# Performance work log

Hardware: AMD Instinct MI355X
Metric: run time of the kernel (lower is better)

## Reference

```python
import jax, jax.numpy as jnp
import numpy as np

NKV = 8      # n_head_kv
G = 8        # n_head // n_head_kv
D = 64       # head_dim (hardcoded in source views)
NH = NKV * G # n_head = 64


def rotate_half(x):
    x1, x2 = x[..., : D // 2], x[..., D // 2:]
    return jnp.concatenate((-x2, x1), axis=-1)


def setup_inputs() -> dict:
    key = jax.random.key(0)
    ks = jax.random.split(key, 9)
    B, S, H = 2, 1024, 4096
    hidden_states = jax.random.normal(ks[0], (B, S, H), dtype=jnp.float32)
    alibi = jnp.zeros((B * NH, 1, S), dtype=jnp.float32)            # unused in this forward path
    attention_mask = jnp.zeros((B, 1, S, S), dtype=jnp.float32)      # unused (is_causal=True)
    cos = jax.random.uniform(ks[1], (S, D), dtype=jnp.float32, minval=-1.0, maxval=1.0)
    sin = jax.random.uniform(ks[2], (S, D), dtype=jnp.float32, minval=-1.0, maxval=1.0)
    wq = jax.random.normal(ks[3], (H, H), dtype=jnp.float32) * 0.02          # Linear weight (out, in)
    wk = jax.random.normal(ks[4], (NKV * D, H), dtype=jnp.float32) * 0.02
    wv = jax.random.normal(ks[5], (NKV * D, H), dtype=jnp.float32) * 0.02
    wd = jax.random.normal(ks[6], (H, H), dtype=jnp.float32) * 0.02          # dense weight
    return {"hidden_states": hidden_states, "alibi": alibi, "attention_mask": attention_mask,
            "cos": cos, "sin": sin, "wq": wq, "wk": wk, "wv": wv, "wd": wd}


def reference(hidden_states, alibi, attention_mask, cos, sin, wq, wk, wv, wd):
    B, S, H = hidden_states.shape
    # fused-style projections (Linear: x @ W.T, no bias)
    # q: [B, S, NKV, G, D] -> [B, NKV, G, S, D]; head h = kv_group*G + j (group-major, matches source rearrange)
    q = (hidden_states @ wq.T).reshape(B, S, NKV, G, D).transpose(0, 2, 3, 1, 4)
    k = (hidden_states @ wk.T).reshape(B, S, NKV, D).transpose(0, 2, 1, 3)   # [B, NKV, S, D]
    v = (hidden_states @ wv.T).reshape(B, S, NKV, D).transpose(0, 2, 1, 3)
    # RoPE (cos/sin broadcast over batch/head dims)
    q = q * cos + rotate_half(q) * sin
    k = k * cos + rotate_half(k) * sin
    # grouped-query attention without materializing broadcast K/V
    inv_norm = jnp.asarray(1.0 / np.sqrt(D), dtype=hidden_states.dtype)
    scores = jnp.einsum('bkgsd,bktd->bkgst', q, k) * inv_norm        # [B, NKV, G, S, S]
    causal = jnp.tril(jnp.ones((S, S), dtype=bool))
    neg = jnp.finfo(scores.dtype).min
    scores = jnp.where(causal, scores, scores + neg)
    probs = jax.nn.softmax(scores, axis=-1)
    out = jnp.einsum('bkgst,bktd->bkgsd', probs, v)                  # [B, NKV, G, S, D]
    out = out.reshape(B, NH, S, D).transpose(0, 2, 1, 3).reshape(B, S, NH * D)
    return out @ wd.T
```

## Files before the change

### kernel.cpp

```cpp
#include <hip/hip_runtime.h>
#include <hip/hip_bf16.h>
#include <cstdint>

typedef short short8 __attribute__((ext_vector_type(8)));
typedef __bf16 bf16x8 __attribute__((ext_vector_type(8)));
typedef float float4v __attribute__((ext_vector_type(4)));
typedef float float16v __attribute__((ext_vector_type(16)));

#define NKV 8
#define G 8
#define D 64
#define NH 64
#define BB 2
#define S 1024
#define H 4096
#define MROWS (BB*S)
#define NQKV (H + 2*NKV*D)

__device__ __forceinline__ unsigned short f2b(float f) {
    union { float f; uint32_t u; } v; v.f = f;
    uint32_t u = v.u;
    uint32_t r = (u + 0x7FFFu + ((u >> 16) & 1u)) >> 16;
    return (unsigned short)r;
}
__device__ __forceinline__ float b2f(unsigned short b) {
    union { float f; uint32_t u; } v; v.u = ((uint32_t)b) << 16;
    return v.f;
}
__device__ __forceinline__ unsigned short f2b_n(float f) {
    union { __bf16 h; unsigned short u; } v; v.h = (__bf16)f;
    return v.u;
}

__device__ __forceinline__ void gload_lds16(const unsigned short* g, unsigned short* l) {
    __builtin_amdgcn_global_load_lds(
        (const __attribute__((address_space(1))) uint32_t*)g,
        (__attribute__((address_space(3))) uint32_t*)l, 16, 0, 0);
}

__global__ void cvt_all(const float* __restrict__ hs, const float* __restrict__ wq,
                        const float* __restrict__ wk, const float* __restrict__ wv,
                        const float* __restrict__ wd,
                        unsigned short* __restrict__ hs_b, unsigned short* __restrict__ wqkv_b,
                        unsigned short* __restrict__ wd_b) {
    const size_t N0 = (size_t)MROWS * H;
    const size_t N1 = (size_t)H * H;
    const size_t N2 = (size_t)512 * H;
    const size_t N3 = (size_t)512 * H;
    const size_t N4 = (size_t)H * H;
    const size_t total4 = (N0 + N1 + N2 + N3 + N4) / 4;
    size_t i = (size_t)blockIdx.x * blockDim.x + threadIdx.x;
    const size_t stride = (size_t)gridDim.x * blockDim.x;
    for (; i < total4; i += stride) {
        size_t e = i * 4;
        const float* s; unsigned short* d;
        if (e < N0)                { s = hs + e;                  d = hs_b + e; }
        else if (e < N0+N1)        { s = wq + (e-N0);             d = wqkv_b + (e-N0); }
        else if (e < N0+N1+N2)     { s = wk + (e-N0-N1);          d = wqkv_b + N1 + (e-N0-N1); }
        else if (e < N0+N1+N2+N3)  { s = wv + (e-N0-N1-N2);       d = wqkv_b + N1+N2 + (e-N0-N1-N2); }
        else                       { s = wd + (e-N0-N1-N2-N3);    d = wd_b + (e-N0-N1-N2-N3); }
        float4 f = *(const float4*)s;
        ushort4 o;
        o.x = f2b(f.x); o.y = f2b(f.y); o.z = f2b(f.z); o.w = f2b(f.w);
        *(ushort4*)d = o;
    }
}

template <int MODE>
__global__ __launch_bounds__(256) void gemm_nt(
    const unsigned short* __restrict__ A, const unsigned short* __restrict__ W,
    void* __restrict__ Cv, int M, int N, int K,
    const float* __restrict__ cosb, const float* __restrict__ sinb,
    unsigned short* __restrict__ qa, unsigned short* __restrict__ ka,
    unsigned short* __restrict__ vt) {
    __shared__ unsigned short sh[17408];
    unsigned short* As = sh;
    unsigned short* Bs = sh + 4096;
    const int bm = blockIdx.y * 128, bn = blockIdx.x * 128;
    const int tid = threadIdx.x;
    const int w = tid >> 6, lane = tid & 63;
    const int n32 = lane & 31, khalf = lane >> 5;
    const int wm = (w & 1) * 64, wn = (w >> 1) * 64;

    const int r0 = tid >> 2;
    const int c0 = (tid & 3) ^ ((r0 >> 2) & 3);
    const unsigned short* pA0 = A + (size_t)(bm + r0) * K + c0 * 8;
    const unsigned short* pA1 = A + (size_t)(bm + r0 + 64) * K + c0 * 8;
    const unsigned short* pW0 = W + (size_t)(bn + r0) * K + c0 * 8;
    const unsigned short* pW1 = W + (size_t)(bn + r0 + 64) * K + c0 * 8;
    unsigned short* Asl0 = As + tid * 8;
    unsigned short* Asl1 = As + 2048 + tid * 8;
    unsigned short* Bsl0 = Bs + tid * 8;
    unsigned short* Bsl1 = Bs + 2048 + tid * 8;

    const unsigned short* aP[2][2];
    const unsigned short* bP[2][2];
#pragma unroll
    for (int g = 0; g < 2; g++)
#pragma unroll
        for (int s = 0; s < 2; s++) {
            int cp = ((s << 1) | khalf) ^ ((n32 >> 2) & 3);
            aP[g][s] = &As[(wm + g * 32 + n32) * 32 + cp * 8];
            bP[g][s] = &Bs[(wn + g * 32 + n32) * 32 + cp * 8];
        }

    float16v acc[2][2] = {};

    const int iters = K >> 5;
    for (int it = 0; it < iters; ++it) {
        __syncthreads();
        gload_lds16(pA0, Asl0);
        gload_lds16(pA1, Asl1);
        gload_lds16(pW0, Bsl0);
        gload_lds16(pW1, Bsl1);
        pA0 += 32; pA1 += 32; pW0 += 32; pW1 += 32;
        __syncthreads();
        bf16x8 af[2][2], bf[2][2];
#pragma unroll
        for (int g = 0; g < 2; g++)
#pragma unroll
            for (int s = 0; s < 2; s++) {
                af[g][s] = *(const bf16x8*)aP[g][s];
                bf[g][s] = *(const bf16x8*)bP[g][s];
            }
#pragma unroll
        for (int s = 0; s < 2; s++)
#pragma unroll
            for (int mg = 0; mg < 2; mg++)
#pragma unroll
                for (int ng = 0; ng < 2; ng++)
                    acc[mg][ng] = __builtin_amdgcn_mfma_f32_32x32x16_bf16(
                        af[mg][s], bf[ng][s], acc[mg][ng], 0, 0, 0);
    }

    if (MODE == 0) {
#pragma unroll
        for (int mg = 0; mg < 2; mg++) {
#pragma unroll
            for (int ng = 0; ng < 2; ng++) {
                int gcol = bn + wn + ng * 32 + n32;
#pragma unroll
                for (int reg = 0; reg < 16; reg++) {
                    int grow = bm + wm + mg * 32 + (reg & 3) + 8 * (reg >> 2) + 4 * khalf;
                    ((float*)Cv)[(size_t)grow * N + gcol] = acc[mg][ng][reg];
                }
            }
        }
    } else {
        const int colbase = bn + wn;
        const float SCQ = 0.125f * 1.44269504089f;
        if (bn < H + 512) {
#pragma unroll
            for (int mg = 0; mg < 2; mg++) {
#pragma unroll
                for (int reg = 0; reg < 16; reg++) {
                    int grow = bm + wm + mg * 32 + (reg & 3) + 8 * (reg >> 2) + 4 * khalf;
                    int s = grow & 1023, b = grow >> 10;
                    float x0 = acc[mg][0][reg], x1 = acc[mg][1][reg];
                    float c0  = cosb[s * 64 + n32],      sn0 = sinb[s * 64 + n32];
                    float c1  = cosb[s * 64 + 32 + n32], sn1 = sinb[s * 64 + 32 + n32];
                    float y0 = x0 * c0 - x1 * sn0;
                    float y1 = x1 * c1 + x0 * sn1;
                    unsigned short* dp;
                    if (bn < H) {
                        y0 *= SCQ; y1 *= SCQ;
                        dp = qa + (size_t)(b * 64 + (colbase >> 6)) * (S * D) + s * 64 + n32;
                    } else {
                        dp = ka + (size_t)(b * 8 + ((colbase - H) >> 6)) * (S * D) + s * 64 + n32;
                    }
                    dp[0] = f2b(y0); dp[32] = f2b(y1);
                }
            }
        } else {
            __syncthreads();
#pragma unroll
            for (int mg = 0; mg < 2; mg++)
#pragma unroll
                for (int ng = 0; ng < 2; ng++)
#pragma unroll
                    for (int reg = 0; reg < 16; reg++) {
                        int cl = wn + ng * 32 + n32;
                        int rl = wm + mg * 32 + (reg & 3) + 8 * (reg >> 2) + 4 * khalf;
                        sh[cl * 136 + rl] = f2b(acc[mg][ng][reg]);
                    }
            __syncthreads();
            {
                const int bb = bm >> 10, s0 = bm & 1023;
                const int kv0 = (bn - (H + 512)) >> 6;
                const int cl = tid >> 1, shalf = (tid & 1) * 64;
                const int kv = kv0 + (cl >> 6), dd = cl & 63;
                unsigned short* dstp = vt + (size_t)(bb * 8 + kv) * (D * S)
                                          + (size_t)dd * S + s0 + shalf;
                const unsigned short* srcp = sh + cl * 136 + shalf;
#pragma unroll
                for (int j = 0; j < 8; j++)
                    *(short8*)(dstp + j * 8) = *(const short8*)(srcp + j * 8);
            }
        }
    }
}

__global__ __launch_bounds__(256, 2) void attn_kernel(
    const unsigned short* __restrict__ qa, const unsigned short* __restrict__ ka,
    const unsigned short* __restrict__ vt, unsigned short* __restrict__ out) {
    __shared__ unsigned short Ps[4 * 16 * 72];
    const int p = blockIdx.x;
    const int yy = blockIdx.y;
    const int b = yy >> 5, kvh = (yy >> 2) & 7, gp = yy & 3;
    const int h0 = b * 64 + kvh * 8 + gp * 2;
    const int tid = threadIdx.x, w = tid >> 6, lane = tid & 63;
    const int col = lane & 15, quad = lane >> 4;
    const unsigned short* Kg = ka + (size_t)(b * NKV + kvh) * (S * D);
    const unsigned short* Vg = vt + (size_t)(b * NKV + kvh) * (D * S);
    float4v zero4 = {0.f, 0.f, 0.f, 0.f};

    const int qt0 = p, qt1 = 15 - p;
    const int qb[2] = {qt0 * 64, qt1 * 64};

    bf16x8 aq[2][2][2];
#pragma unroll
    for (int part = 0; part < 2; part++)
#pragma unroll
        for (int hd = 0; hd < 2; hd++)
#pragma unroll
            for (int c = 0; c < 2; c++)
                aq[part][hd][c] = *(const bf16x8*)&qa[(size_t)(h0 + hd) * (S * D)
                                    + (size_t)qb[part] * D + (w * 16 + col) * 64 + c * 32 + quad * 8];

    float l_run[2][2][4] = {};
    float4v o_acc[2][2][4];
#pragma unroll
    for (int part = 0; part < 2; part++)
#pragma unroll
        for (int hd = 0; hd < 2; hd++)
#pragma unroll
            for (int dg = 0; dg < 4; dg++) o_acc[part][hd][dg] = zero4;

    for (int kt = 0; kt <= qt1; kt++) {
        const int kb = kt * 64;
        bf16x8 bk[4][2], bv[4][2];
#pragma unroll
        for (int n16 = 0; n16 < 4; n16++) {
            const unsigned short* kr = &Kg[(size_t)(kb + n16 * 16 + col) * 64 + quad * 8];
            bk[n16][0] = *(const bf16x8*)kr;
            bk[n16][1] = *(const bf16x8*)(kr + 32);
        }
#pragma unroll
        for (int dg = 0; dg < 4; dg++) {
            const unsigned short* vr = &Vg[(size_t)(dg * 16 + col) * S + kb + quad * 8];
            bv[dg][0] = *(const bf16x8*)vr;
            bv[dg][1] = *(const bf16x8*)(vr + 32);
        }

#pragma unroll
        for (int part = 0; part < 2; part++) {
            const int qtp = part ? qt1 : qt0;
            if (kt > qtp) continue;
#pragma unroll
            for (int hd = 0; hd < 2; hd++) {
                float4v sc[4];
                __builtin_amdgcn_s_setprio(1);
#pragma unroll
                for (int n16 = 0; n16 < 4; n16++) {
                    float4v a = __builtin_amdgcn_mfma_f32_16x16x32_bf16(aq[part][hd][0], bk[n16][0], zero4, 0, 0, 0);
                    sc[n16] = __builtin_amdgcn_mfma_f32_16x16x32_bf16(aq[part][hd][1], bk[n16][1], a, 0, 0, 0);
                }
                __builtin_amdgcn_s_setprio(0);
                if (kt == qtp) {
#pragma unroll
                    for (int n16 = 0; n16 < 4; n16++) {
                        int keyl = n16 * 16 + col;
#pragma unroll
                        for (int r = 0; r < 4; r++) {
                            int qrl = w * 16 + quad * 4 + r;
                            sc[n16][r] = (keyl <= qrl) ? sc[n16][r] : -1e30f;
                        }
                    }
                }
#pragma unroll
                for (int n16 = 0; n16 < 4; n16++)
#pragma unroll
                    for (int r = 0; r < 4; r++) {
                        float pr = __builtin_amdgcn_exp2f(sc[n16][r]);
                        sc[n16][r] = pr;
                        l_run[part][hd][r] += pr;
                        Ps[w * 1152 + (quad * 4 + r) * 72 + n16 * 16 + col] = f2b_n(pr);
                    }
                bf16x8 ap[2];
#pragma unroll
                for (int c = 0; c < 2; c++)
                    ap[c] = *(const bf16x8*)&Ps[w * 1152 + col * 72 + c * 32 + quad * 8];
                __builtin_amdgcn_s_setprio(1);
#pragma unroll
                for (int dg = 0; dg < 4; dg++) {
                    float4v t = __builtin_amdgcn_mfma_f32_16x16x32_bf16(ap[0], bv[dg][0], o_acc[part][hd][dg], 0, 0, 0);
                    o_acc[part][hd][dg] = __builtin_amdgcn_mfma_f32_16x16x32_bf16(ap[1], bv[dg][1], t, 0, 0, 0);
                }
                __builtin_amdgcn_s_setprio(0);
            }
        }
    }

#pragma unroll
    for (int part = 0; part < 2; part++)
#pragma unroll
        for (int hd = 0; hd < 2; hd++) {
            const int hcol = ((h0 + hd) & 63) * 64;
#pragma unroll
            for (int r = 0; r < 4; r++) {
                float lsum = l_run[part][hd][r];
#pragma unroll
                for (int off = 1; off < 16; off <<= 1) lsum += __shfl_xor(lsum, off);
                float inv = 1.f / lsum;
                int grow = b * S + qb[part] + w * 16 + quad * 4 + r;
#pragma unroll
                for (int dg = 0; dg < 4; dg++)
                    out[(size_t)grow * H + hcol + dg * 16 + col] = f2b_n(o_acc[part][hd][dg][r] * inv);
            }
        }
}

extern "C" void kernel_launch(void* const* d_in, const int* in_sizes, int n_in,
                              void* d_out, int out_size, void* d_ws, size_t ws_size,
                              hipStream_t stream) {
    const float* hs   = (const float*)d_in[0];
    const float* cosb = (const float*)d_in[3];
    const float* sinb = (const float*)d_in[4];
    const float* wq   = (const float*)d_in[5];
    const float* wk   = (const float*)d_in[6];
    const float* wv   = (const float*)d_in[7];
    const float* wd   = (const float*)d_in[8];

    char* p = (char*)d_ws;
    auto alloc = [&](size_t bytes) { char* r = p; p += (bytes + 255) & ~(size_t)255; return r; };
    unsigned short* wqkv_b = (unsigned short*)alloc((size_t)NQKV * H * 2);
    unsigned short* wd_b   = (unsigned short*)alloc((size_t)H * H * 2);
    unsigned short* qa     = (unsigned short*)alloc((size_t)BB * NH * S * D * 2);
    unsigned short* ka     = (unsigned short*)alloc((size_t)BB * NKV * S * D * 2);
    unsigned short* vt     = (unsigned short*)alloc((size_t)BB * NKV * S * D * 2);
    unsigned short* hs_b   = (unsigned short*)alloc((size_t)MROWS * H * 2);
    unsigned short* ao     = hs_b;

    cvt_all<<<4096, 256, 0, stream>>>(hs, wq, wk, wv, wd, hs_b, wqkv_b, wd_b);

    gemm_nt<1><<<dim3(NQKV / 128, MROWS / 128), 256, 0, stream>>>(
        hs_b, wqkv_b, nullptr, MROWS, NQKV, H, cosb, sinb, qa, ka, vt);
    attn_kernel<<<dim3(8, 64), 256, 0, stream>>>(qa, ka, vt, ao);
    gemm_nt<0><<<dim3(H / 128, MROWS / 128), 256, 0, stream>>>(
        ao, wd_b, d_out, MROWS, H, H, nullptr, nullptr, nullptr, nullptr, nullptr);
}
```

Before: 473.2 us.

## Double-buffer K/V tiles in LDS with async global-to-LDS loads in attention

```diff
diff --git a/kernel.cpp b/kernel.cpp
--- a/kernel.cpp
+++ b/kernel.cpp
@@ -203,6 +203,7 @@
 __global__ __launch_bounds__(256, 2) void attn_kernel(
     const unsigned short* __restrict__ qa, const unsigned short* __restrict__ ka,
     const unsigned short* __restrict__ vt, unsigned short* __restrict__ out) {
+    __shared__ unsigned short KV[2][8192];
     __shared__ unsigned short Ps[4 * 16 * 72];
     const int p = blockIdx.x;
     const int yy = blockIdx.y;
@@ -214,6 +215,15 @@
     const unsigned short* Vg = vt + (size_t)(b * NKV + kvh) * (D * S);
     float4v zero4 = {0.f, 0.f, 0.f, 0.f};
 
+    const int sr = tid >> 3;
+    const int scs = ((tid & 7) ^ (sr & 7)) * 8;
+
+#define ATTN_STAGE(BUF, KB) { \
+    gload_lds16(Kg + (size_t)((KB) + sr) * 64 + scs,      &KV[BUF][tid * 8]); \
+    gload_lds16(Kg + (size_t)((KB) + sr + 32) * 64 + scs, &KV[BUF][2048 + tid * 8]); \
+    gload_lds16(Vg + (size_t)sr * S + (KB) + scs,         &KV[BUF][4096 + tid * 8]); \
+    gload_lds16(Vg + (size_t)(sr + 32) * S + (KB) + scs,  &KV[BUF][6144 + tid * 8]); }
+
     const int qt0 = p, qt1 = 15 - p;
     const int qb[2] = {qt0 * 64, qt1 * 64};
 
@@ -236,20 +246,32 @@
 #pragma unroll
             for (int dg = 0; dg < 4; dg++) o_acc[part][hd][dg] = zero4;
 
+    ATTN_STAGE(0, 0)
+    asm volatile("s_waitcnt vmcnt(0)" ::: "memory");
+    __builtin_amdgcn_s_barrier();
+
     for (int kt = 0; kt <= qt1; kt++) {
-        const int kb = kt * 64;
+        const int cur = kt & 1;
+        const int knext = ((kt < qt1) ? kt + 1 : qt1) * 64;
+        ATTN_STAGE(cur ^ 1, knext)
+        asm volatile("s_waitcnt vmcnt(4)" ::: "memory");
+        __builtin_amdgcn_s_barrier();
+        __builtin_amdgcn_sched_barrier(0);
+
+        const unsigned short* Kl = KV[cur];
+        const unsigned short* Vl = KV[cur] + 4096;
         bf16x8 bk[4][2], bv[4][2];
 #pragma unroll
         for (int n16 = 0; n16 < 4; n16++) {
-            const unsigned short* kr = &Kg[(size_t)(kb + n16 * 16 + col) * 64 + quad * 8];
-            bk[n16][0] = *(const bf16x8*)kr;
-            bk[n16][1] = *(const bf16x8*)(kr + 32);
+            const int R = n16 * 16 + col, x = R & 7;
+            bk[n16][0] = *(const bf16x8*)&Kl[R * 64 + (quad ^ x) * 8];
+            bk[n16][1] = *(const bf16x8*)&Kl[R * 64 + ((quad + 4) ^ x) * 8];
         }
 #pragma unroll
         for (int dg = 0; dg < 4; dg++) {
-            const unsigned short* vr = &Vg[(size_t)(dg * 16 + col) * S + kb + quad * 8];
-            bv[dg][0] = *(const bf16x8*)vr;
-            bv[dg][1] = *(const bf16x8*)(vr + 32);
+            const int R = dg * 16 + col, x = R & 7;
+            bv[dg][0] = *(const bf16x8*)&Vl[R * 64 + (quad ^ x) * 8];
+            bv[dg][1] = *(const bf16x8*)&Vl[R * 64 + ((quad + 4) ^ x) * 8];
         }
 
 #pragma unroll
@@ -299,6 +321,8 @@
                 __builtin_amdgcn_s_setprio(0);
             }
         }
+        __builtin_amdgcn_sched_barrier(0);
+        __builtin_amdgcn_s_barrier();
     }
 
 #pragma unroll
@@ -318,6 +342,7 @@
                     out[(size_t)grow * H + hcol + dg * 16 + col] = f2b_n(o_acc[part][hd][dg][r] * inv);
             }
         }
+#undef ATTN_STAGE
 }
 
 extern "C" void kernel_launch(void* const* d_in, const int* in_sizes, int n_in,
```

After: 443.2 us, median of 2. -6.3%, faster.
